# Kernel optimization log

Hardware: AMD Instinct MI355X
Metric: run time of the kernel (lower is better)

Reference implementation:

```python
import jax, jax.numpy as jnp
import numpy as np

N_HEADS = 16

def setup_inputs() -> dict:
    key = jax.random.key(0)
    kx, kk, kq, kv, ko = jax.random.split(key, 5)
    B, T, D = 8, 1024, 1024
    s = 1.0 / np.sqrt(D)
    return {
        'x':  jax.random.normal(kx, (B, T, D), dtype=jnp.float32),
        'Wk': jax.random.normal(kk, (D, D), dtype=jnp.float32) * s,
        'Wq': jax.random.normal(kq, (D, D), dtype=jnp.float32) * s,
        'Wv': jax.random.normal(kv, (D, D), dtype=jnp.float32) * s,
        'Wo': jax.random.normal(ko, (D, D), dtype=jnp.float32) * s,
    }

def reference(x, Wk, Wq, Wv, Wo):
    B, T, D = x.shape
    H = D // N_HEADS  # head dim
    # projections (nn.Linear with bias=False: y = x @ W^T)
    k = (x @ Wk.T).reshape(B, T, N_HEADS, H).transpose(0, 2, 1, 3)  # [B,n,T,H]
    q = (x @ Wq.T).reshape(B, T, N_HEADS, H).transpose(0, 2, 1, 3)
    v = (x @ Wv.T).reshape(B, T, N_HEADS, H).transpose(0, 2, 1, 3)
    scores = jnp.einsum('bnqh,bnkh->bnqk', q, k)                    # [B,n,T,T]
    causal = jnp.tril(jnp.ones((T, T), dtype=bool))
    # original: masked_fill(-inf) BEFORE scaling; -inf/sqrt(H) stays -inf
    scores = jnp.where(causal, scores, -jnp.inf) / jnp.sqrt(jnp.float32(H))
    att = jax.nn.softmax(scores, axis=-1)
    # dropout p=0.0 -> identity
    out = jnp.einsum('bnqk,bnkh->bnqh', att, v)                     # [B,n,T,H]
    out = out.transpose(0, 2, 1, 3).reshape(B, T, D)
    return out @ Wo.T
```

## Files before the change

kernel.cpp:

```cpp
#include <hip/hip_runtime.h>
#include <stdint.h>

typedef __bf16 bf16x8 __attribute__((ext_vector_type(8)));
typedef float f32x4 __attribute__((ext_vector_type(4)));
typedef unsigned short ushort_t;
typedef unsigned int uint_t;

__device__ inline ushort_t f2bf(float f) {
  uint_t u = __builtin_bit_cast(uint_t, f);
  u = (u + 0x7FFFu + ((u >> 16) & 1u)) >> 16;
  return (ushort_t)u;
}

__device__ inline void gll16(const void* g, void* l) {
  __builtin_amdgcn_global_load_lds(
      (__attribute__((address_space(1))) void*)(uintptr_t)g,
      (__attribute__((address_space(3))) void*)(uint32_t)(uintptr_t)l,
      16, 0, 0);
}

__global__ void cast_all(const float* __restrict__ x, const float* __restrict__ w0,
                         const float* __restrict__ w1, const float* __restrict__ w2,
                         const float* __restrict__ w3, ushort_t* __restrict__ xb,
                         ushort_t* __restrict__ wc, float s0) {
  const int i = blockIdx.x * 256 + threadIdx.x;
  const float* src;
  ushort_t* dst;
  float sc = 1.0f;
  int j;
  if (i < (1 << 21)) {
    src = x;
    dst = xb;
    j = i;
  } else {
    const int k = i - (1 << 21);
    const int which = k >> 18;
    src = which == 0 ? w0 : which == 1 ? w1 : which == 2 ? w2 : w3;
    if (which == 0) sc = s0;
    dst = wc + (k >> 18) * (1 << 20);
    j = k & 0x3FFFF;
  }
  float4 v = reinterpret_cast<const float4*>(src)[j];
  ushort4 o;
  o.x = f2bf(v.x * sc);
  o.y = f2bf(v.y * sc);
  o.z = f2bf(v.z * sc);
  o.w = f2bf(v.w * sc);
  reinterpret_cast<ushort4*>(dst)[j] = o;
}

#define MFMA16(A_, B_, C_) __builtin_amdgcn_mfma_f32_16x16x32_bf16(A_, B_, C_, 0, 0, 0)
#define SBAR __builtin_amdgcn_s_barrier
#define LGKM0 asm volatile("s_waitcnt lgkmcnt(0)" ::: "memory")

template <int MF, int NF, int NTN, int LDC, bool F32OUT>
__global__ __launch_bounds__(512, 2) void gemm8p(const ushort_t* __restrict__ A,
                                                 const ushort_t* __restrict__ B,
                                                 void* __restrict__ C) {
  constexpr int BM = MF * 32;
  constexpr int BN = NF * 64;
  constexpr int NA = BM / 64;
  constexpr int NB = BN / 64;
  constexpr int NB0 = (NB >= 2) ? NB / 2 : 1;
  constexpr int NG0 = (NF >= 2) ? NF / 2 : 1;
  constexpr int AU = BM * 64;
  constexpr int BUF = AU + BN * 64;
  constexpr int NWG = (8192 / BM) * NTN;
  __shared__ __attribute__((aligned(16))) ushort_t smem[2 * BUF];

  const int tid = threadIdx.x;
  const int lane = tid & 63;
  const int w = tid >> 6;
  const int wm = w >> 2, wn = w & 3;

  const int bid = blockIdx.x;
  const int swz = (bid & 7) * (NWG / 8) + (bid >> 3);
  const int m0 = (swz / NTN) * BM;
  const int n0 = (swz % NTN) * BN;

  const int scol = ((tid & 7) ^ ((tid >> 3) & 7)) * 8;
  const ushort_t* gA = A + (size_t)(m0 + (tid >> 3)) * 1024 + scol;
  const ushort_t* gB = B + (size_t)(n0 + (tid >> 3)) * 1024 + scol;

  const int lr = lane & 15;
  const int hi = lane >> 4;
  const int arow = (wm * MF * 16 + lr) * 64;
  const int brow = AU + (wn * NF * 16 + lr) * 64;
  const int cx0 = (hi * 8) ^ ((lane & 7) << 3);
  const int cx1 = cx0 ^ 32;

  f32x4 acc[MF][NF] = {};
  bf16x8 a[MF / 2][2];
  bf16x8 b[NF][2];

  auto stage_a_even = [&](int wbu, int sk) __attribute__((always_inline)) {
    if constexpr (MF == 8) {
      gll16(gA + 0 * 65536 + sk, &smem[wbu + 0 * 4096 + (w << 9)]);
      gll16(gA + 2 * 65536 + sk, &smem[wbu + 2 * 4096 + (w << 9)]);
    } else {
#pragma unroll
      for (int i = 0; i < NA; ++i)
        gll16(gA + i * 65536 + sk, &smem[wbu + i * 4096 + (w << 9)]);
    }
  };
  auto stage_a_odd = [&](int wbu, int sk) __attribute__((always_inline)) {
    if constexpr (MF == 8) {
      gll16(gA + 1 * 65536 + sk, &smem[wbu + 1 * 4096 + (w << 9)]);
      gll16(gA + 3 * 65536 + sk, &smem[wbu + 3 * 4096 + (w << 9)]);
    }
  };
  auto stage_b0 = [&](int wbu, int sk) __attribute__((always_inline)) {
#pragma unroll
    for (int i = 0; i < NB0; ++i)
      gll16(gB + i * 65536 + sk, &smem[wbu + AU + i * 4096 + (w << 9)]);
  };
  auto stage_b1 = [&](int wbu, int sk) __attribute__((always_inline)) {
#pragma unroll
    for (int i = NB0; i < NB; ++i)
      gll16(gB + i * 65536 + sk, &smem[wbu + AU + i * 4096 + (w << 9)]);
  };
  auto rdA = [&](int rbu, int mbase) __attribute__((always_inline)) {
#pragma unroll
    for (int m = 0; m < MF / 2; ++m) {
      const int base = rbu + arow + (mbase + m) * 1024;
      a[m][0] = *(const bf16x8*)&smem[base + cx0];
      a[m][1] = *(const bf16x8*)&smem[base + cx1];
    }
  };
  auto rdBg = [&](int rbu, int ng0, int ng1) __attribute__((always_inline)) {
#pragma unroll
    for (int n = 0; n < NF; ++n) {
      if (n < ng0 || n >= ng1) continue;
      const int base = rbu + brow + n * 1024;
      b[n][0] = *(const bf16x8*)&smem[base + cx0];
      b[n][1] = *(const bf16x8*)&smem[base + cx1];
    }
  };
  auto mmg = [&](int mbase, int ng0, int ng1) __attribute__((always_inline)) {
#pragma unroll
    for (int m = 0; m < MF / 2; ++m)
#pragma unroll
      for (int n = 0; n < NF; ++n) {
        if (n < ng0 || n >= ng1) continue;
        acc[mbase + m][n] = MFMA16(a[m][0], b[n][0], acc[mbase + m][n]);
        acc[mbase + m][n] = MFMA16(a[m][1], b[n][1], acc[mbase + m][n]);
      }
  };

  auto tile = [&](int rbu, int wbu, int sk, bool pf) __attribute__((always_inline)) {
    if (pf) {
      stage_a_even(wbu, sk);
      if constexpr (MF == 8)
        asm volatile("s_waitcnt vmcnt(4)" ::: "memory");
      else
        asm volatile("s_waitcnt vmcnt(2)" ::: "memory");
    } else {
      if constexpr (MF == 8)
        asm volatile("s_waitcnt vmcnt(2)" ::: "memory");
      else
        asm volatile("s_waitcnt vmcnt(0)" ::: "memory");
    }
    SBAR();
    rdA(rbu, 0);
    rdBg(rbu, 0, NG0);
    LGKM0;
    __builtin_amdgcn_s_setprio(1);
    mmg(0, 0, NG0);
    __builtin_amdgcn_s_setprio(0);
    SBAR();
    rdBg(rbu, NG0, NF);
    if (pf) stage_b0(wbu, sk);
    SBAR();
    LGKM0;
    __builtin_amdgcn_s_setprio(1);
    mmg(0, NG0, NF);
    __builtin_amdgcn_s_setprio(0);
    SBAR();
    if (pf) {
      stage_b1(wbu, sk);
      if constexpr (MF == 8)
        asm volatile("s_waitcnt vmcnt(5)" ::: "memory");
    } else {
      if constexpr (MF == 8)
        asm volatile("s_waitcnt vmcnt(0)" ::: "memory");
    }
    SBAR();
    rdA(rbu, MF / 2);
    LGKM0;
    __builtin_amdgcn_s_setprio(1);
    mmg(MF / 2, NG0, NF);
    __builtin_amdgcn_s_setprio(0);
    SBAR();
    if (pf) stage_a_odd(wbu, sk);
    SBAR();
    __builtin_amdgcn_s_setprio(1);
    mmg(MF / 2, 0, NG0);
    __builtin_amdgcn_s_setprio(0);
    SBAR();
  };

  stage_a_even(0, 0);
  stage_b0(0, 0);
  stage_b1(0, 0);
  stage_a_odd(0, 0);
  int sk = 64;
  for (int it = 0; it < 7; ++it) {
    tile(0, BUF, sk, true);
    sk += 64;
    tile(BUF, 0, sk, true);
    sk += 64;
  }
  tile(0, BUF, sk, true);
  tile(BUF, 0, 0, false);

  const size_t erow = (size_t)(m0 + wm * MF * 16 + hi * 4);
  const int ecol = n0 + wn * NF * 16 + lr;
#pragma unroll
  for (int mf = 0; mf < MF; ++mf)
#pragma unroll
    for (int nf = 0; nf < NF; ++nf)
#pragma unroll
      for (int r = 0; r < 4; ++r) {
        const size_t idx = (erow + mf * 16 + r) * LDC + ecol + nf * 16;
        if constexpr (F32OUT)
          ((float*)C)[idx] = acc[mf][nf][r];
        else
          ((ushort_t*)C)[idx] = f2bf(acc[mf][nf][r]);
      }
}

__global__ __launch_bounds__(256, 2) void attn_fwd(const ushort_t* __restrict__ QKV,
                                                   ushort_t* __restrict__ ctx) {
  const int bid = blockIdx.x;
  const int h = bid & 15;
  const int b = (bid >> 4) & 7;
  const int p = bid >> 7;
  const int tid = threadIdx.x;
  const int lane = tid & 63;
  const int w = tid >> 6;
  const int lr = lane & 15;
  const int lg = lane >> 4;
  const int dk = lg << 3;

  __shared__ __attribute__((aligned(16))) ushort_t Ks[2][64 * 72];
  __shared__ __attribute__((aligned(16))) uint_t VtDw[2][64 * 36];

  const int kkey = tid >> 2, kdg = tid & 3;
  const int vkp = tid & 31, vdg = tid >> 5;
  const int pkp = ((vkp >> 4) << 4) | (((vkp >> 1) & 3) << 2) |
                  (((vkp >> 3) & 1) << 1) | (vkp & 1);
  const ushort_t* kgbase =
      QKV + ((size_t)(b * 1024 + kkey)) * 3072 + 1024 + h * 64 + kdg * 16;
  const ushort_t* vgbase =
      QKV + ((size_t)(b * 1024 + 2 * vkp)) * 3072 + 2048 + h * 64 + vdg * 8;

  const float FMAX2 = 23.083120654223414f;

  const int qtA = p, qtB = 7 - p;
  const int ntB = (qtB + 1) << 1;
  const int wrow0A = (qtA << 7) + w * 32;
  const int wrow0B = (qtB << 7) + w * 32;

  bf16x8 qfA[2][2], qfB[2][2];
#pragma unroll
  for (int i = 0; i < 2; ++i) {
    const ushort_t* qpA =
        QKV + ((size_t)(b * 1024 + wrow0A + i * 16 + lr)) * 3072 + h * 64 + dk;
    qfA[i][0] = *reinterpret_cast<const bf16x8*>(qpA);
    qfA[i][1] = *reinterpret_cast<const bf16x8*>(qpA + 32);
    const ushort_t* qpB =
        QKV + ((size_t)(b * 1024 + wrow0B + i * 16 + lr)) * 3072 + h * 64 + dk;
    qfB[i][0] = *reinterpret_cast<const bf16x8*>(qpB);
    qfB[i][1] = *reinterpret_cast<const bf16x8*>(qpB + 32);
  }

  f32x4 oA[2][4] = {}, oB[2][4] = {};
  float lsA[2] = {0.f, 0.f}, lsB[2] = {0.f, 0.f};

  uint4 rk0 = *reinterpret_cast<const uint4*>(kgbase);
  uint4 rk1 = *reinterpret_cast<const uint4*>(kgbase + 8);
  uint4 rv0 = *reinterpret_cast<const uint4*>(vgbase);
  uint4 rv1 = *reinterpret_cast<const uint4*>(vgbase + 3072);

  for (int t = 0; t < ntB; ++t) {
    const int bsel = t & 1;
    asm volatile("s_waitcnt vmcnt(0)" ::: "memory");
    {
      uint_t* kd = reinterpret_cast<uint_t*>(&Ks[bsel][kkey * 72 + kdg * 16]);
      *reinterpret_cast<uint4*>(kd) = rk0;
      *reinterpret_cast<uint4*>(kd + 4) = rk1;
      const ushort_t* e0 = reinterpret_cast<const ushort_t*>(&rv0);
      const ushort_t* e1 = reinterpret_cast<const ushort_t*>(&rv1);
#pragma unroll
      for (int j = 0; j < 8; ++j)
        VtDw[bsel][(vdg * 8 + j) * 36 + pkp] = (uint_t)e0[j] | ((uint_t)e1[j] << 16);
    }
    if (t + 1 < ntB) {
      const size_t off = (size_t)(t + 1) * 64 * 3072;
      rk0 = *reinterpret_cast<const uint4*>(kgbase + off);
      rk1 = *reinterpret_cast<const uint4*>(kgbase + off + 8);
      rv0 = *reinterpret_cast<const uint4*>(vgbase + off);
      rv1 = *reinterpret_cast<const uint4*>(vgbase + off + 3072);
    }
    asm volatile("s_waitcnt lgkmcnt(0)" ::: "memory");
    __builtin_amdgcn_s_barrier();

    const int kb = t << 6;
    const bool actB = (kb <= wrow0B + 31);
    const bool actA = (kb <= wrow0A + 31);
    if (!(actA || actB)) continue;

    bf16x8 kf0[4], kf1[4];
#pragma unroll
    for (int f = 0; f < 4; ++f) {
      kf0[f] = *reinterpret_cast<const bf16x8*>(&Ks[bsel][(f * 16 + lr) * 72 + dk]);
      kf1[f] =
          *reinterpret_cast<const bf16x8*>(&Ks[bsel][(f * 16 + lr) * 72 + 32 + dk]);
    }
    bf16x8 vb[2][4];
#pragma unroll
    for (int kblk = 0; kblk < 2; ++kblk)
#pragma unroll
      for (int fh = 0; fh < 4; ++fh)
        vb[kblk][fh] = *reinterpret_cast<const bf16x8*>(
            &VtDw[bsel][(fh * 16 + lr) * 36 + kblk * 16 + (lg << 2)]);

    auto group = [&](const bf16x8(&qf)[2][2], f32x4(&o)[2][4], float(&ls)[2],
                     int wrow0) __attribute__((always_inline)) {
      f32x4 s[2][4];
      __builtin_amdgcn_s_setprio(1);
#pragma unroll
      for (int i = 0; i < 2; ++i)
#pragma unroll
        for (int f = 0; f < 4; ++f) {
          f32x4 z = {0.f, 0.f, 0.f, 0.f};
          z = __builtin_amdgcn_mfma_f32_16x16x32_bf16(kf0[f], qf[i][0], z, 0, 0, 0);
          s[i][f] = __builtin_amdgcn_mfma_f32_16x16x32_bf16(kf1[f], qf[i][1], z, 0, 0, 0);
        }
      __builtin_amdgcn_s_setprio(0);
      const bool needmask = (kb + 63 > wrow0);
#pragma unroll
      for (int i = 0; i < 2; ++i) {
        const int qr = wrow0 + i * 16 + lr;
        uint_t d0[4], d1[4];
#pragma unroll
        for (int f = 0; f < 4; ++f) {
          const int kbase = kb + f * 16 + (lg << 2);
          float p0 = __builtin_amdgcn_exp2f(s[i][f][0] - FMAX2);
          float p1 = __builtin_amdgcn_exp2f(s[i][f][1] - FMAX2);
          float p2 = __builtin_amdgcn_exp2f(s[i][f][2] - FMAX2);
          float p3 = __builtin_amdgcn_exp2f(s[i][f][3] - FMAX2);
          if (needmask) {
            p0 = (kbase + 0 <= qr) ? p0 : 0.f;
            p1 = (kbase + 1 <= qr) ? p1 : 0.f;
            p2 = (kbase + 2 <= qr) ? p2 : 0.f;
            p3 = (kbase + 3 <= qr) ? p3 : 0.f;
          }
          ls[i] += (p0 + p1) + (p2 + p3);
          asm("v_cvt_pk_bf16_f32 %0, %1, %2" : "=v"(d0[f]) : "v"(p0), "v"(p1));
          asm("v_cvt_pk_bf16_f32 %0, %1, %2" : "=v"(d1[f]) : "v"(p2), "v"(p3));
        }
        __builtin_amdgcn_s_setprio(1);
#pragma unroll
        for (int kblk = 0; kblk < 2; ++kblk) {
          uint4 paw;
          paw.x = d0[2 * kblk];
          paw.y = d1[2 * kblk];
          paw.z = d0[2 * kblk + 1];
          paw.w = d1[2 * kblk + 1];
          const bf16x8 pa = __builtin_bit_cast(bf16x8, paw);
#pragma unroll
          for (int fh = 0; fh < 4; ++fh)
            o[i][fh] = __builtin_amdgcn_mfma_f32_16x16x32_bf16(pa, vb[kblk][fh],
                                                               o[i][fh], 0, 0, 0);
        }
        __builtin_amdgcn_s_setprio(0);
      }
    };

    if (actB) group(qfB, oB, lsB, wrow0B);
    if (actA) group(qfA, oA, lsA, wrow0A);
  }

  auto epi = [&](f32x4(&o)[2][4], float(&ls)[2], int wrow0)
      __attribute__((always_inline)) {
#pragma unroll
    for (int i = 0; i < 2; ++i) {
      float s = ls[i];
      s += __shfl_xor(s, 16);
      s += __shfl_xor(s, 32);
      const float linv = 1.0f / s;
      const size_t crow = (size_t)(b * 1024 + wrow0 + i * 16 + (lg << 2));
#pragma unroll
      for (int r = 0; r < 4; ++r) {
        const float li = __shfl(linv, (lg << 2) + r);
#pragma unroll
        for (int fh = 0; fh < 4; ++fh)
          ctx[(crow + r) * 1024 + h * 64 + fh * 16 + lr] = f2bf(o[i][fh][r] * li);
      }
    }
  };
  epi(oB, lsB, wrow0B);
  epi(oA, lsA, wrow0A);
}

extern "C" void kernel_launch(void* const* d_in, const int* in_sizes, int n_in,
                              void* d_out, int out_size, void* d_ws, size_t ws_size,
                              hipStream_t stream) {
  const float* x = (const float*)d_in[0];
  const float* Wk = (const float*)d_in[1];
  const float* Wq = (const float*)d_in[2];
  const float* Wv = (const float*)d_in[3];
  const float* Wo = (const float*)d_in[4];

  char* ws = (char*)d_ws;
  ushort_t* xb = (ushort_t*)ws;
  ushort_t* Wc = (ushort_t*)(ws + (16u << 20));
  ushort_t* Wob = Wc + 3u * 1024 * 1024;
  ushort_t* QKV = (ushort_t*)(ws + (24u << 20));
  ushort_t* ctx = xb;

  cast_all<<<12288, 256, 0, stream>>>(x, Wq, Wk, Wv, Wo, xb, Wc,
                                      0.125f * 1.4426950408889634f);

  gemm8p<8, 3, 16, 3072, false><<<512, 512, 0, stream>>>(xb, Wc, QKV);

  attn_fwd<<<512, 256, 0, stream>>>(QKV, ctx);

  gemm8p<4, 2, 8, 1024, true><<<512, 512, 0, stream>>>(ctx, Wob, (float*)d_out);
}
```

Baseline: 125.9 us.

## Simplify GEMM mainloop to a single-barrier double-buffered schedule

```diff
diff --git a/kernel.cpp b/kernel.cpp
--- a/kernel.cpp
+++ b/kernel.cpp
@@ -51,7 +51,7 @@
 
 #define MFMA16(A_, B_, C_) __builtin_amdgcn_mfma_f32_16x16x32_bf16(A_, B_, C_, 0, 0, 0)
 #define SBAR __builtin_amdgcn_s_barrier
-#define LGKM0 asm volatile("s_waitcnt lgkmcnt(0)" ::: "memory")
+#define SCHED0 __builtin_amdgcn_sched_barrier(0)
 
 template <int MF, int NF, int NTN, int LDC, bool F32OUT>
 __global__ __launch_bounds__(512, 2) void gemm8p(const ushort_t* __restrict__ A,
@@ -61,8 +61,6 @@
   constexpr int BN = NF * 64;
   constexpr int NA = BM / 64;
   constexpr int NB = BN / 64;
-  constexpr int NB0 = (NB >= 2) ? NB / 2 : 1;
-  constexpr int NG0 = (NF >= 2) ? NF / 2 : 1;
   constexpr int AU = BM * 64;
   constexpr int BUF = AU + BN * 64;
   constexpr int NWG = (8192 / BM) * NTN;
@@ -90,119 +88,67 @@
   const int cx1 = cx0 ^ 32;
 
   f32x4 acc[MF][NF] = {};
-  bf16x8 a[MF / 2][2];
+  bf16x8 a0[MF / 2][2], a1[MF / 2][2];
   bf16x8 b[NF][2];
 
-  auto stage_a_even = [&](int wbu, int sk) __attribute__((always_inline)) {
-    if constexpr (MF == 8) {
-      gll16(gA + 0 * 65536 + sk, &smem[wbu + 0 * 4096 + (w << 9)]);
-      gll16(gA + 2 * 65536 + sk, &smem[wbu + 2 * 4096 + (w << 9)]);
-    } else {
-#pragma unroll
-      for (int i = 0; i < NA; ++i)
-        gll16(gA + i * 65536 + sk, &smem[wbu + i * 4096 + (w << 9)]);
-    }
-  };
-  auto stage_a_odd = [&](int wbu, int sk) __attribute__((always_inline)) {
-    if constexpr (MF == 8) {
-      gll16(gA + 1 * 65536 + sk, &smem[wbu + 1 * 4096 + (w << 9)]);
-      gll16(gA + 3 * 65536 + sk, &smem[wbu + 3 * 4096 + (w << 9)]);
-    }
-  };
-  auto stage_b0 = [&](int wbu, int sk) __attribute__((always_inline)) {
-#pragma unroll
-    for (int i = 0; i < NB0; ++i)
+  auto stage_all = [&](int wbu, int sk) __attribute__((always_inline)) {
+#pragma unroll
+    for (int i = 0; i < NA; ++i)
+      gll16(gA + i * 65536 + sk, &smem[wbu + i * 4096 + (w << 9)]);
+#pragma unroll
+    for (int i = 0; i < NB; ++i)
       gll16(gB + i * 65536 + sk, &smem[wbu + AU + i * 4096 + (w << 9)]);
   };
-  auto stage_b1 = [&](int wbu, int sk) __attribute__((always_inline)) {
-#pragma unroll
-    for (int i = NB0; i < NB; ++i)
-      gll16(gB + i * 65536 + sk, &smem[wbu + AU + i * 4096 + (w << 9)]);
-  };
-  auto rdA = [&](int rbu, int mbase) __attribute__((always_inline)) {
+  auto rdA = [&](int rbu, int mbase, bf16x8(&aa)[MF / 2][2])
+      __attribute__((always_inline)) {
 #pragma unroll
     for (int m = 0; m < MF / 2; ++m) {
       const int base = rbu + arow + (mbase + m) * 1024;
-      a[m][0] = *(const bf16x8*)&smem[base + cx0];
-      a[m][1] = *(const bf16x8*)&smem[base + cx1];
-    }
-  };
-  auto rdBg = [&](int rbu, int ng0, int ng1) __attribute__((always_inline)) {
+      aa[m][0] = *(const bf16x8*)&smem[base + cx0];
+      aa[m][1] = *(const bf16x8*)&smem[base + cx1];
+    }
+  };
+  auto rdBall = [&](int rbu) __attribute__((always_inline)) {
 #pragma unroll
     for (int n = 0; n < NF; ++n) {
-      if (n < ng0 || n >= ng1) continue;
       const int base = rbu + brow + n * 1024;
       b[n][0] = *(const bf16x8*)&smem[base + cx0];
       b[n][1] = *(const bf16x8*)&smem[base + cx1];
     }
   };
-  auto mmg = [&](int mbase, int ng0, int ng1) __attribute__((always_inline)) {
+  auto mmH = [&](int mbase, bf16x8(&aa)[MF / 2][2]) __attribute__((always_inline)) {
 #pragma unroll
     for (int m = 0; m < MF / 2; ++m)
 #pragma unroll
       for (int n = 0; n < NF; ++n) {
-        if (n < ng0 || n >= ng1) continue;
-        acc[mbase + m][n] = MFMA16(a[m][0], b[n][0], acc[mbase + m][n]);
-        acc[mbase + m][n] = MFMA16(a[m][1], b[n][1], acc[mbase + m][n]);
+        acc[mbase + m][n] = MFMA16(aa[m][0], b[n][0], acc[mbase + m][n]);
+        acc[mbase + m][n] = MFMA16(aa[m][1], b[n][1], acc[mbase + m][n]);
       }
   };
 
   auto tile = [&](int rbu, int wbu, int sk, bool pf) __attribute__((always_inline)) {
-    if (pf) {
-      stage_a_even(wbu, sk);
-      if constexpr (MF == 8)
-        asm volatile("s_waitcnt vmcnt(4)" ::: "memory");
-      else
-        asm volatile("s_waitcnt vmcnt(2)" ::: "memory");
-    } else {
-      if constexpr (MF == 8)
-        asm volatile("s_waitcnt vmcnt(2)" ::: "memory");
-      else
-        asm volatile("s_waitcnt vmcnt(0)" ::: "memory");
-    }
+    rdA(rbu, 0, a0);
+    rdBall(rbu);
+    if (pf) stage_all(wbu, sk);
+    rdA(rbu, MF / 2, a1);
+    SCHED0;
+    __builtin_amdgcn_s_setprio(1);
+    mmH(0, a0);
+    __builtin_amdgcn_s_setprio(0);
+    SCHED0;
+    __builtin_amdgcn_s_setprio(1);
+    mmH(MF / 2, a1);
+    __builtin_amdgcn_s_setprio(0);
+    SCHED0;
+    if (pf) asm volatile("s_waitcnt vmcnt(0)" ::: "memory");
     SBAR();
-    rdA(rbu, 0);
-    rdBg(rbu, 0, NG0);
-    LGKM0;
-    __builtin_amdgcn_s_setprio(1);
-    mmg(0, 0, NG0);
-    __builtin_amdgcn_s_setprio(0);
-    SBAR();
-    rdBg(rbu, NG0, NF);
-    if (pf) stage_b0(wbu, sk);
-    SBAR();
-    LGKM0;
-    __builtin_amdgcn_s_setprio(1);
-    mmg(0, NG0, NF);
-    __builtin_amdgcn_s_setprio(0);
-    SBAR();
-    if (pf) {
-      stage_b1(wbu, sk);
-      if constexpr (MF == 8)
-        asm volatile("s_waitcnt vmcnt(5)" ::: "memory");
-    } else {
-      if constexpr (MF == 8)
-        asm volatile("s_waitcnt vmcnt(0)" ::: "memory");
-    }
-    SBAR();
-    rdA(rbu, MF / 2);
-    LGKM0;
-    __builtin_amdgcn_s_setprio(1);
-    mmg(MF / 2, NG0, NF);
-    __builtin_amdgcn_s_setprio(0);
-    SBAR();
-    if (pf) stage_a_odd(wbu, sk);
-    SBAR();
-    __builtin_amdgcn_s_setprio(1);
-    mmg(MF / 2, 0, NG0);
-    __builtin_amdgcn_s_setprio(0);
-    SBAR();
-  };
-
-  stage_a_even(0, 0);
-  stage_b0(0, 0);
-  stage_b1(0, 0);
-  stage_a_odd(0, 0);
+    SCHED0;
+  };
+
+  stage_all(0, 0);
+  asm volatile("s_waitcnt vmcnt(0)" ::: "memory");
+  SBAR();
+  SCHED0;
   int sk = 64;
   for (int it = 0; it < 7; ++it) {
     tile(0, BUF, sk, true);
```

New measurement: 123.3 us. -2.1%, faster.
